# Kernel tuning notes

Hardware: AMD Instinct MI355X
Metric: run time of the kernel (lower is better)

Reference implementation:

```python
import jax, jax.numpy as jnp
import numpy as np

EPS = 1e-5

def _conv_bn_relu(x, w, gamma, beta):
    # x: [B, C, N], w: [O, C] (1x1 conv, no bias)
    y = jnp.einsum('oc,bcn->bon', w, x)
    # BatchNorm1d in training mode: per-channel stats over (B, N)
    mean = jnp.mean(y, axis=(0, 2), keepdims=True)
    var = jnp.var(y, axis=(0, 2), keepdims=True)
    yhat = (y - mean) * jax.lax.rsqrt(var + EPS)
    return jax.nn.relu(gamma[None, :, None] * yhat + beta[None, :, None])


def setup_inputs() -> dict:
    key = jax.random.key(0)
    ks = jax.random.split(key, 8)
    B, C, N, Cr = 4, 256, 4096, 32
    x = jax.random.normal(ks[0], (B, C, N), dtype=jnp.float32)
    w1 = jax.random.normal(ks[1], (Cr, C), dtype=jnp.float32) * (1.0 / np.sqrt(C))
    w2 = jax.random.normal(ks[2], (Cr, C), dtype=jnp.float32) * (1.0 / np.sqrt(C))
    w3 = jax.random.normal(ks[3], (C, C), dtype=jnp.float32) * (1.0 / np.sqrt(C))
    g1 = 1.0 + 0.1 * jax.random.normal(ks[4], (Cr,), dtype=jnp.float32)
    b1 = 0.1 * jax.random.normal(ks[5], (Cr,), dtype=jnp.float32)
    g2 = 1.0 + 0.1 * jax.random.normal(ks[6], (Cr,), dtype=jnp.float32)
    b2 = 0.1 * jax.random.normal(ks[7], (Cr,), dtype=jnp.float32)
    g3 = jnp.ones((C,), dtype=jnp.float32)
    b3 = jnp.zeros((C,), dtype=jnp.float32)
    return {'x': x, 'w1': w1, 'w2': w2, 'w3': w3,
            'g1': g1, 'b1': b1, 'g2': g2, 'b2': b2, 'g3': g3, 'b3': b3}


def reference(x, w1, w2, w3, g1, b1, g2, b2, g3, b3):
    # a: [B, N, Cr] (queries), k: [B, Cr, N] (keys)
    a = _conv_bn_relu(x, w1, g1, b1).transpose(0, 2, 1)
    k = _conv_bn_relu(x, w2, g2, b2)
    # s[b, n, m] = softmax_m(sum_c a[b,n,c] * k[b,c,m])
    s = jax.nn.softmax(jnp.einsum('bnc,bcm->bnm', a, k), axis=-1)
    d = _conv_bn_relu(x, w3, g3, b3)  # [B, C, N]
    # out = x + d @ s^T : out[b,c,m] = sum_n d[b,c,n] * s[m,n]
    out = x + jnp.einsum('bcn,bmn->bcm', d, s)
    return out
```

## Files before the change

### kernel.cpp

```cpp
#include <hip/hip_runtime.h>
#include <cstddef>
#include <cstdint>

#define B_ 4
#define C_ 256
#define N_ 4096
#define KF_OFF_B  ((size_t)1024 * 1024)
#define DF_OFF_B  ((size_t)2 * 1024 * 1024)
#define SUM_OFF_B ((size_t)10 * 1024 * 1024)
#define ML_OFF_B  (SUM_OFF_B + 1280 * 4)
#define XH_OFF_B  (ML_OFF_B + 524288)
#define XL_OFF_B  (XH_OFF_B + (size_t)8 * 1024 * 1024)
#define WH_OFF_B  (XL_OFF_B + (size_t)8 * 1024 * 1024)
#define WL_OFF_B  (WH_OFF_B + 163840)
#define LOG2E 1.4426950408889634f

typedef unsigned short bfraw;
typedef __attribute__((ext_vector_type(8))) short short8;
typedef __attribute__((ext_vector_type(4))) float float4v;
typedef __attribute__((ext_vector_type(4))) bfraw bfraw4;

__device__ inline bfraw f2bf(float f) {
    union { float f; uint32_t u; } c; c.f = f;
    uint32_t u = c.u;
    u += 0x7fffu + ((u >> 16) & 1u);
    return (bfraw)(u >> 16);
}
__device__ inline float bf2f(bfraw h) {
    union { uint32_t u; float f; } c; c.u = ((uint32_t)h) << 16;
    return c.f;
}
#if __has_builtin(__builtin_amdgcn_exp2f)
__device__ inline float EXP2(float x) { return __builtin_amdgcn_exp2f(x); }
#else
__device__ inline float EXP2(float x) { return exp2f(x); }
#endif
__device__ inline uint32_t pack2(float a, float b) {
    union { float f; uint32_t u; } ca, cb; ca.f = a; cb.f = b;
#if __has_builtin(__builtin_amdgcn_perm)
    return __builtin_amdgcn_perm(cb.u + 0x8000u, ca.u + 0x8000u, 0x07060302u);
#else
    return ((ca.u + 0x8000u) >> 16) | ((cb.u + 0x8000u) & 0xffff0000u);
#endif
}

__global__ void zero_kernel(float* __restrict__ sums) {
    for (int i = threadIdx.x; i < 640; i += 256) sums[i] = 0.f;
}

__global__ __launch_bounds__(256) void wsplit_kernel(
    const float* __restrict__ w1, const float* __restrict__ w2,
    const float* __restrict__ w3, uint8_t* __restrict__ wsb)
{
    bfraw* wh = (bfraw*)(wsb + WH_OFF_B);
    bfraw* wl = (bfraw*)(wsb + WL_OFF_B);
    int idx4 = (blockIdx.x * 256 + threadIdx.x) * 4;
    int ch = idx4 >> 8, k = idx4 & 255;
    const float* wr = (ch < 32) ? (w1 + ch * C_)
                      : (ch < 64) ? (w2 + (ch - 32) * C_)
                                  : (w3 + (ch - 64) * C_);
    float4 v = *(const float4*)&wr[k];
    float va[4] = {v.x, v.y, v.z, v.w};
    bfraw4 h, l;
#pragma unroll
    for (int j = 0; j < 4; ++j) {
        h[j] = f2bf(va[j]);
        l[j] = f2bf(va[j] - bf2f(h[j]));
    }
    *(bfraw4*)&wh[idx4] = h;
    *(bfraw4*)&wl[idx4] = l;
}

__global__ __launch_bounds__(256) void xtsplit_kernel(
    const float* __restrict__ x, uint8_t* __restrict__ wsb)
{
    __shared__ float Ls[64][65];
    bfraw* xh = (bfraw*)(wsb + XH_OFF_B);
    bfraw* xl = (bfraw*)(wsb + XL_OFF_B);
    const int id = blockIdx.x;
    const int b  = id >> 8;
    const int c0 = ((id >> 6) & 3) << 6;
    const int n0 = (id & 63) << 6;
    const int t  = threadIdx.x;
    {
        int cl = t >> 4, nc = (t & 15) << 2;
#pragma unroll
        for (int i = 0; i < 4; ++i) {
            float4 v = *(const float4*)&x[((size_t)b * C_ + c0 + cl + i * 16) * N_ + n0 + nc];
            Ls[cl + i * 16][nc + 0] = v.x;
            Ls[cl + i * 16][nc + 1] = v.y;
            Ls[cl + i * 16][nc + 2] = v.z;
            Ls[cl + i * 16][nc + 3] = v.w;
        }
    }
    __syncthreads();
    int nl = t >> 2, seg = t & 3;
    bfraw hb[16], lb[16];
#pragma unroll
    for (int j = 0; j < 16; ++j) {
        float v = Ls[seg * 16 + j][nl];
        bfraw h = f2bf(v);
        hb[j] = h;
        lb[j] = f2bf(v - bf2f(h));
    }
    size_t base = ((size_t)b * N_ + n0 + nl) * 256 + c0 + seg * 16;
    *(short8*)&xh[base]     = *(short8*)&hb[0];
    *(short8*)&xh[base + 8] = *(short8*)&hb[8];
    *(short8*)&xl[base]     = *(short8*)&lb[0];
    *(short8*)&xl[base + 8] = *(short8*)&lb[8];
}

__global__ __launch_bounds__(256, 2) void ygemm_kernel(uint8_t* __restrict__ wsb)
{
    const bfraw* xh = (const bfraw*)(wsb + XH_OFF_B);
    const bfraw* xl = (const bfraw*)(wsb + XL_OFF_B);
    const bfraw* wh = (const bfraw*)(wsb + WH_OFF_B);
    const bfraw* wl = (const bfraw*)(wsb + WL_OFF_B);
    bfraw* qf  = (bfraw*)wsb;
    bfraw* kfp = (bfraw*)(wsb + KF_OFF_B);
    bfraw* dfp = (bfraw*)(wsb + DF_OFF_B);
    float* sums  = (float*)(wsb + SUM_OFF_B);
    float* sumsq = sums + 320;
    __shared__ float redS[4][64], redQ[4][64];

    const int bx = blockIdx.x;
    const int by = blockIdx.y;
    const int b  = bx >> 5;
    const int n0 = (bx << 7) & (N_ - 1);
    const int t = threadIdx.x, w = t >> 6, l = t & 63, lq = l & 15, lg = l >> 4;
    const int nw = n0 + w * 32;

    float4v acc[4][2];
#pragma unroll
    for (int i = 0; i < 4; ++i)
#pragma unroll
        for (int j = 0; j < 2; ++j) acc[i][j] = (float4v){0.f, 0.f, 0.f, 0.f};

    for (int s = 0; s < 8; ++s) {
        const int k0 = s * 32;
        short8 ah[4], al[4], bh[2], bl[2];
#pragma unroll
        for (int ct = 0; ct < 4; ++ct) {
            size_t off = (size_t)(by * 64 + ct * 16 + lq) * 256 + k0 + lg * 8;
            ah[ct] = *(const short8*)&wh[off];
            al[ct] = *(const short8*)&wl[off];
        }
#pragma unroll
        for (int nt = 0; nt < 2; ++nt) {
            size_t off = ((size_t)b * N_ + nw + nt * 16 + lq) * 256 + k0 + lg * 8;
            bh[nt] = *(const short8*)&xh[off];
            bl[nt] = *(const short8*)&xl[off];
        }
#pragma unroll
        for (int ct = 0; ct < 4; ++ct)
#pragma unroll
            for (int nt = 0; nt < 2; ++nt) {
                acc[ct][nt] = __builtin_amdgcn_mfma_f32_16x16x32_bf16(ah[ct], bh[nt], acc[ct][nt], 0, 0, 0);
                acc[ct][nt] = __builtin_amdgcn_mfma_f32_16x16x32_bf16(al[ct], bh[nt], acc[ct][nt], 0, 0, 0);
                acc[ct][nt] = __builtin_amdgcn_mfma_f32_16x16x32_bf16(ah[ct], bl[nt], acc[ct][nt], 0, 0, 0);
            }
    }
#pragma unroll
    for (int ct = 0; ct < 4; ++ct) {
        float sv[4], qv[4];
#pragma unroll
        for (int r = 0; r < 4; ++r) {
            float a0 = acc[ct][0][r], a1 = acc[ct][1][r];
            sv[r] = a0 + a1;
            qv[r] = a0 * a0 + a1 * a1;
#pragma unroll
            for (int m = 1; m < 16; m <<= 1) {
                sv[r] += __shfl_xor(sv[r], m);
                qv[r] += __shfl_xor(qv[r], m);
            }
        }
        if (lq == 0) {
#pragma unroll
            for (int r = 0; r < 4; ++r) {
                redS[w][ct * 16 + lg * 4 + r] = sv[r];
                redQ[w][ct * 16 + lg * 4 + r] = qv[r];
            }
        }
    }
    __syncthreads();
    if (t < 64) {
        float s = redS[0][t] + redS[1][t] + redS[2][t] + redS[3][t];
        float q = redQ[0][t] + redQ[1][t] + redQ[2][t] + redQ[3][t];
        atomicAdd(&sums[by * 64 + t], s);
        atomicAdd(&sumsq[by * 64 + t], q);
    }
    if (by == 0) {
#pragma unroll
        for (int ct = 0; ct < 4; ++ct)
#pragma unroll
            for (int nt = 0; nt < 2; ++nt)
#pragma unroll
                for (int r = 0; r < 4; ++r) {
                    int c = ct * 16 + lg * 4 + r;
                    int n = nw + nt * 16 + lq;
                    size_t addr = ((size_t)(b << 8) + (n >> 4)) * 512
                                + (size_t)(((n & 15) | (((c >> 3) & 3) << 4)) << 3) + (c & 7);
                    bfraw v = f2bf(acc[ct][nt][r]);
                    if (c < 32) qf[addr] = v; else kfp[addr] = v;
                }
    } else {
#pragma unroll
        for (int ct = 0; ct < 4; ++ct)
#pragma unroll
            for (int nt = 0; nt < 2; ++nt)
#pragma unroll
                for (int r = 0; r < 4; ++r) {
                    int cg = (by - 1) * 64 + ct * 16 + lg * 4 + r;
                    int n = nw + nt * 16 + lq;
                    size_t addr = (((size_t)(b << 4) + (cg >> 4)) * 128 + (n >> 5)) * 512
                                + (size_t)(((cg & 15) | (((n >> 3) & 3) << 4)) << 3) + (n & 7);
                    dfp[addr] = f2bf(acc[ct][nt][r]);
                }
    }
}

__global__ void finalize_kernel(
    const float* __restrict__ g1, const float* __restrict__ b1,
    const float* __restrict__ g2, const float* __restrict__ b2,
    const float* __restrict__ g3, const float* __restrict__ b3,
    float* __restrict__ sums)
{
    int ch = threadIdx.x;
    if (ch >= 320) return;
    const float inv = 1.0f / (float)(B_ * N_);
    float mean = sums[ch] * inv;
    float var = sums[320 + ch] * inv - mean * mean;
    float g, bb;
    if (ch < 32)      { g = g1[ch];      bb = b1[ch]; }
    else if (ch < 64) { g = g2[ch - 32]; bb = b2[ch - 32]; }
    else              { g = g3[ch - 64]; bb = b3[ch - 64]; }
    float sc = g * rsqrtf(var + 1e-5f);
    float bi = bb - sc * mean;
    if (ch < 32) { sc *= LOG2E; bi *= LOG2E; }
    sums[640 + ch] = sc;
    sums[960 + ch] = bi;
}

__global__ __launch_bounds__(256) void affine_kernel(uint8_t* __restrict__ wsb)
{
    bfraw* base = (bfraw*)wsb;
    const float* sc = (const float*)(wsb + SUM_OFF_B) + 640;
    const float* bi = sc + 320;
    size_t i8 = ((size_t)blockIdx.x * 256 + threadIdx.x) * 8;
    bfraw4 v0 = *(bfraw4*)&base[i8];
    bfraw4 v1 = *(bfraw4*)&base[i8 + 4];
    if (i8 < 1048576) {
        int ch0 = (((int)(i8 >> 7)) & 3) * 8 + ((i8 < 524288) ? 0 : 32);
        float4 s0 = *(const float4*)&sc[ch0];
        float4 s1 = *(const float4*)&sc[ch0 + 4];
        float4 c0 = *(const float4*)&bi[ch0];
        float4 c1 = *(const float4*)&bi[ch0 + 4];
        float sa[8] = {s0.x, s0.y, s0.z, s0.w, s1.x, s1.y, s1.z, s1.w};
        float ca[8] = {c0.x, c0.y, c0.z, c0.w, c1.x, c1.y, c1.z, c1.w};
#pragma unroll
        for (int j = 0; j < 4; ++j) {
            v0[j] = f2bf(fmaxf(0.f, fmaf(sa[j],     bf2f(v0[j]), ca[j])));
            v1[j] = f2bf(fmaxf(0.f, fmaf(sa[j + 4], bf2f(v1[j]), ca[j + 4])));
        }
    } else {
        size_t rel = i8 - 1048576;
        int ch = 64 + (((int)(rel >> 16)) & 15) * 16 + (((int)(rel >> 3)) & 15);
        float s = sc[ch], b = bi[ch];
#pragma unroll
        for (int j = 0; j < 4; ++j) {
            v0[j] = f2bf(fmaxf(0.f, fmaf(s, bf2f(v0[j]), b)));
            v1[j] = f2bf(fmaxf(0.f, fmaf(s, bf2f(v1[j]), b)));
        }
    }
    *(bfraw4*)&base[i8] = v0;
    *(bfraw4*)&base[i8 + 4] = v1;
}

__global__ __launch_bounds__(256, 4) void mlpass_kernel(uint8_t* __restrict__ wsb)
{
    const bfraw* qf  = (const bfraw*)wsb;
    const bfraw* kfp = (const bfraw*)(wsb + KF_OFF_B);
    float* mpart = (float*)(wsb + ML_OFF_B);
    float* lpart = mpart + 65536;
    const int id = blockIdx.x;
    const int b = id & 3;
    const int ks = (id >> 2) & 3;
    const int n0q = (id >> 4) << 6;
    const int tid = threadIdx.x;
    const int w = tid >> 6, l = tid & 63, lq = l & 15, lg = l >> 4;
    const short8 qfrag = *(const short8*)&qf[((size_t)(b * 256 + (n0q >> 4) + w)) * 512 + l * 8];

    float mx = -1e30f, sum = 0.f;
    const int tbeg = b * 256 + ks * 64;
    for (int tk = tbeg; tk < tbeg + 64; tk += 8) {
        float4v st[8];
#pragma unroll
        for (int kt = 0; kt < 8; ++kt) {
            short8 kf = *(const short8*)&kfp[((size_t)(tk + kt)) * 512 + l * 8];
            float4v z = {0.f, 0.f, 0.f, 0.f};
            st[kt] = __builtin_amdgcn_mfma_f32_16x16x32_bf16(kf, qfrag, z, 0, 0, 0);
        }
        float m1 = st[0][0];
#pragma unroll
        for (int kt = 0; kt < 8; ++kt)
#pragma unroll
            for (int r = 0; r < 4; ++r) m1 = fmaxf(m1, st[kt][r]);
        float nm = fmaxf(mx, m1);
        float ae = 0.f;
#pragma unroll
        for (int kt = 0; kt < 8; ++kt)
#pragma unroll
            for (int r = 0; r < 4; ++r) ae += EXP2(st[kt][r] - nm);
        sum = sum * EXP2(mx - nm) + ae;
        mx = nm;
    }
#pragma unroll
    for (int m = 16; m < 64; m <<= 1) {
        float mo = __shfl_xor(mx, m);
        float so = __shfl_xor(sum, m);
        float nm = fmaxf(mx, mo);
        sum = sum * EXP2(mx - nm) + so * EXP2(mo - nm);
        mx = nm;
    }
    if (lg == 0) {
        int idx = ks * 16384 + b * N_ + n0q + w * 16 + lq;
        mpart[idx] = mx;
        lpart[idx] = sum;
    }
}

__global__ __launch_bounds__(256, 4) void flash_kernel(
    const float* __restrict__ x, const uint8_t* __restrict__ wsb,
    float* __restrict__ out)
{
    const bfraw* qf  = (const bfraw*)wsb;
    const bfraw* kfp = (const bfraw*)(wsb + KF_OFF_B);
    const bfraw* dfp = (const bfraw*)(wsb + DF_OFF_B);
    const float* mpart = (const float*)(wsb + ML_OFF_B);
    const float* lpart = mpart + 65536;
    __shared__ bfraw Pl[2][32 * 128];

    const int id  = blockIdx.x;
    const int b   = id & 3;
    const int hf  = (id >> 2) & 1;
    const int n0q = (id >> 3) << 5;
    const int tid = threadIdx.x;
    const int w   = tid >> 6;
    const int l   = tid & 63;
    const int lq  = l & 15;
    const int lg  = l >> 4;
    const int sw  = lq & 7;
    const int qt_loc = w >> 1;
    const int ks_loc = w & 1;
    const int ctg0 = hf * 8 + w;
    const int ctg1 = hf * 8 + 4 + w;

    const short8 qfrag = *(const short8*)&qf[((size_t)(b * 256 + (n0q >> 4) + qt_loc)) * 512 + l * 8];
    float mlq;
    {
        int qi = b * N_ + n0q + qt_loc * 16 + lq;
        float M = -1e30f, ms[4], ls[4];
#pragma unroll
        for (int s = 0; s < 4; ++s) {
            ms[s] = mpart[s * 16384 + qi];
            ls[s] = lpart[s * 16384 + qi];
            M = fmaxf(M, ms[s]);
        }
        float L = 0.f;
#pragma unroll
        for (int s = 0; s < 4; ++s) L += ls[s] * EXP2(ms[s] - M);
        mlq = M + __log2f(L);
    }

    float4v acc[2][2];
#pragma unroll
    for (int i = 0; i < 2; ++i)
#pragma unroll
        for (int j = 0; j < 2; ++j) acc[i][j] = (float4v){0.f, 0.f, 0.f, 0.f};

    short8 kfr[4], dfr[2][4];
#pragma unroll
    for (int kt = 0; kt < 4; ++kt)
        kfr[kt] = *(const short8*)&kfp[((size_t)(b * 256 + ks_loc * 4 + kt)) * 512 + l * 8];
#pragma unroll
    for (int ch = 0; ch < 4; ++ch) {
        dfr[0][ch] = *(const short8*)&dfp[(((size_t)(b * 16 + ctg0)) * 128 + ch) * 512 + l * 8];
        dfr[1][ch] = *(const short8*)&dfp[(((size_t)(b * 16 + ctg1)) * 128 + ch) * 512 + l * 8];
    }

    const int qrow = qt_loc * 16 + lq;
    for (int it = 0; it < 32; ++it) {
        const int ib = it & 1;
        const int nit = (it + 1) & 31;
        float4v st[4];
#pragma unroll
        for (int kt = 0; kt < 4; ++kt) {
            float4v z = {0.f, 0.f, 0.f, 0.f};
            st[kt] = __builtin_amdgcn_mfma_f32_16x16x32_bf16(kfr[kt], qfrag, z, 0, 0, 0);
        }
#pragma unroll
        for (int kt = 0; kt < 4; ++kt)
            kfr[kt] = *(const short8*)&kfp[((size_t)(b * 256 + nit * 8 + ks_loc * 4 + kt)) * 512 + l * 8];
#pragma unroll
        for (int kt = 0; kt < 4; ++kt) {
            float e0 = EXP2(st[kt][0] - mlq);
            float e1 = EXP2(st[kt][1] - mlq);
            float e2 = EXP2(st[kt][2] - mlq);
            float e3 = EXP2(st[kt][3] - mlq);
            uint2 pd = {pack2(e0, e1), pack2(e2, e3)};
            int g = (2 * (ks_loc * 4 + kt) + (lg >> 1)) ^ sw;
            *(uint2*)&Pl[ib][qrow * 128 + g * 8 + (lg & 1) * 4] = pd;
        }
        __syncthreads();
#pragma unroll
        for (int ch = 0; ch < 4; ++ch) {
            short8 bfr[2];
#pragma unroll
            for (int qt = 0; qt < 2; ++qt) {
                int g = (ch * 4 + lg) ^ sw;
                bfr[qt] = *(const short8*)&Pl[ib][(qt * 16 + lq) * 128 + g * 8];
            }
            acc[0][0] = __builtin_amdgcn_mfma_f32_16x16x32_bf16(dfr[0][ch], bfr[0], acc[0][0], 0, 0, 0);
            acc[0][1] = __builtin_amdgcn_mfma_f32_16x16x32_bf16(dfr[0][ch], bfr[1], acc[0][1], 0, 0, 0);
            acc[1][0] = __builtin_amdgcn_mfma_f32_16x16x32_bf16(dfr[1][ch], bfr[0], acc[1][0], 0, 0, 0);
            acc[1][1] = __builtin_amdgcn_mfma_f32_16x16x32_bf16(dfr[1][ch], bfr[1], acc[1][1], 0, 0, 0);
            dfr[0][ch] = *(const short8*)&dfp[(((size_t)(b * 16 + ctg0)) * 128 + nit * 4 + ch) * 512 + l * 8];
            dfr[1][ch] = *(const short8*)&dfp[(((size_t)(b * 16 + ctg1)) * 128 + nit * 4 + ch) * 512 + l * 8];
        }
    }
#pragma unroll
    for (int ct = 0; ct < 2; ++ct) {
        int ctg = ct ? ctg1 : ctg0;
#pragma unroll
        for (int r = 0; r < 4; ++r) {
            int c = ctg * 16 + lg * 4 + r;
            size_t base = ((size_t)b * C_ + c) * N_ + n0q;
#pragma unroll
            for (int qt = 0; qt < 2; ++qt) {
                size_t idx = base + qt * 16 + lq;
                out[idx] = x[idx] + acc[ct][qt][r];
            }
        }
    }
}

extern "C" void kernel_launch(void* const* d_in, const int* in_sizes, int n_in,
                              void* d_out, int out_size, void* d_ws, size_t ws_size,
                              hipStream_t stream) {
    (void)in_sizes; (void)n_in; (void)out_size; (void)ws_size;
    const float* x  = (const float*)d_in[0];
    const float* w1 = (const float*)d_in[1];
    const float* w2 = (const float*)d_in[2];
    const float* w3 = (const float*)d_in[3];
    const float* g1 = (const float*)d_in[4];
    const float* b1 = (const float*)d_in[5];
    const float* g2 = (const float*)d_in[6];
    const float* b2 = (const float*)d_in[7];
    const float* g3 = (const float*)d_in[8];
    const float* b3 = (const float*)d_in[9];
    uint8_t* wsb = (uint8_t*)d_ws;
    float* sums = (float*)(wsb + SUM_OFF_B);
    float* outp = (float*)d_out;

    zero_kernel<<<1, 256, 0, stream>>>(sums);
    wsplit_kernel<<<80, 256, 0, stream>>>(w1, w2, w3, wsb);
    xtsplit_kernel<<<1024, 256, 0, stream>>>(x, wsb);
    ygemm_kernel<<<dim3(128, 5), 256, 0, stream>>>(wsb);
    finalize_kernel<<<1, 320, 0, stream>>>(g1, b1, g2, b2, g3, b3, sums);
    affine_kernel<<<2560, 256, 0, stream>>>(wsb);
    mlpass_kernel<<<1024, 256, 0, stream>>>(wsb);
    flash_kernel<<<1024, 256, 0, stream>>>(x, wsb, outp);
}
```

Measured before the change: 211.2 us.

## Double query tile per flash block to reuse K/D fragments

Each flash block now handles 64 queries instead of 32. Every loaded K and D fragment feeds twice as many MFMAs, and the grid halves to 512 blocks. The log-sum-exp offset is folded into the MFMA accumulator init so the separate subtract before exp2 goes away, and s_setprio is raised around the MFMA burst. In exchange, register use and LDS usage double (launch bounds drop to 2) and there are fewer blocks to hide latency.

```diff
diff --git a/kernel.cpp b/kernel.cpp
--- a/kernel.cpp
+++ b/kernel.cpp
@@ -329,7 +329,7 @@
     }
 }
 
-__global__ __launch_bounds__(256, 4) void flash_kernel(
+__global__ __launch_bounds__(256, 2) void flash_kernel(
     const float* __restrict__ x, const uint8_t* __restrict__ wsb,
     float* __restrict__ out)
 {
@@ -338,27 +338,30 @@
     const bfraw* dfp = (const bfraw*)(wsb + DF_OFF_B);
     const float* mpart = (const float*)(wsb + ML_OFF_B);
     const float* lpart = mpart + 65536;
-    __shared__ bfraw Pl[2][32 * 128];
+    __shared__ bfraw Pl[2][64 * 128];
 
     const int id  = blockIdx.x;
     const int b   = id & 3;
     const int hf  = (id >> 2) & 1;
-    const int n0q = (id >> 3) << 5;
+    const int n0q = (id >> 3) << 6;
     const int tid = threadIdx.x;
     const int w   = tid >> 6;
     const int l   = tid & 63;
     const int lq  = l & 15;
     const int lg  = l >> 4;
     const int sw  = lq & 7;
-    const int qt_loc = w >> 1;
+    const int qp  = w >> 1;
     const int ks_loc = w & 1;
     const int ctg0 = hf * 8 + w;
     const int ctg1 = hf * 8 + 4 + w;
 
-    const short8 qfrag = *(const short8*)&qf[((size_t)(b * 256 + (n0q >> 4) + qt_loc)) * 512 + l * 8];
-    float mlq;
-    {
-        int qi = b * N_ + n0q + qt_loc * 16 + lq;
+    const short8 qfragA = *(const short8*)&qf[((size_t)(b * 256 + (n0q >> 4) + 2 * qp)) * 512 + l * 8];
+    const short8 qfragB = *(const short8*)&qf[((size_t)(b * 256 + (n0q >> 4) + 2 * qp + 1)) * 512 + l * 8];
+
+    float mlqA, mlqB;
+#pragma unroll
+    for (int qs = 0; qs < 2; ++qs) {
+        int qi = b * N_ + n0q + (2 * qp + qs) * 16 + lq;
         float M = -1e30f, ms[4], ls[4];
 #pragma unroll
         for (int s = 0; s < 4; ++s) {
@@ -369,14 +372,17 @@
         float L = 0.f;
 #pragma unroll
         for (int s = 0; s < 4; ++s) L += ls[s] * EXP2(ms[s] - M);
-        mlq = M + __log2f(L);
-    }
-
-    float4v acc[2][2];
+        float v = M + __log2f(L);
+        if (qs == 0) mlqA = v; else mlqB = v;
+    }
+    const float4v zA = {-mlqA, -mlqA, -mlqA, -mlqA};
+    const float4v zB = {-mlqB, -mlqB, -mlqB, -mlqB};
+
+    float4v acc[2][4];
 #pragma unroll
     for (int i = 0; i < 2; ++i)
 #pragma unroll
-        for (int j = 0; j < 2; ++j) acc[i][j] = (float4v){0.f, 0.f, 0.f, 0.f};
+        for (int j = 0; j < 4; ++j) acc[i][j] = (float4v){0.f, 0.f, 0.f, 0.f};
 
     short8 kfr[4], dfr[2][4];
 #pragma unroll
@@ -388,42 +394,55 @@
         dfr[1][ch] = *(const short8*)&dfp[(((size_t)(b * 16 + ctg1)) * 128 + ch) * 512 + l * 8];
     }
 
-    const int qrow = qt_loc * 16 + lq;
+    const int qrowA = (2 * qp) * 16 + lq;
+    const int qrowB = (2 * qp + 1) * 16 + lq;
     for (int it = 0; it < 32; ++it) {
         const int ib = it & 1;
         const int nit = (it + 1) & 31;
-        float4v st[4];
+        float4v stA[4], stB[4];
 #pragma unroll
         for (int kt = 0; kt < 4; ++kt) {
-            float4v z = {0.f, 0.f, 0.f, 0.f};
-            st[kt] = __builtin_amdgcn_mfma_f32_16x16x32_bf16(kfr[kt], qfrag, z, 0, 0, 0);
+            stA[kt] = __builtin_amdgcn_mfma_f32_16x16x32_bf16(kfr[kt], qfragA, zA, 0, 0, 0);
+            stB[kt] = __builtin_amdgcn_mfma_f32_16x16x32_bf16(kfr[kt], qfragB, zB, 0, 0, 0);
         }
 #pragma unroll
         for (int kt = 0; kt < 4; ++kt)
             kfr[kt] = *(const short8*)&kfp[((size_t)(b * 256 + nit * 8 + ks_loc * 4 + kt)) * 512 + l * 8];
 #pragma unroll
         for (int kt = 0; kt < 4; ++kt) {
-            float e0 = EXP2(st[kt][0] - mlq);
-            float e1 = EXP2(st[kt][1] - mlq);
-            float e2 = EXP2(st[kt][2] - mlq);
-            float e3 = EXP2(st[kt][3] - mlq);
-            uint2 pd = {pack2(e0, e1), pack2(e2, e3)};
             int g = (2 * (ks_loc * 4 + kt) + (lg >> 1)) ^ sw;
-            *(uint2*)&Pl[ib][qrow * 128 + g * 8 + (lg & 1) * 4] = pd;
+            {
+                float e0 = EXP2(stA[kt][0]);
+                float e1 = EXP2(stA[kt][1]);
+                float e2 = EXP2(stA[kt][2]);
+                float e3 = EXP2(stA[kt][3]);
+                uint2 pd = {pack2(e0, e1), pack2(e2, e3)};
+                *(uint2*)&Pl[ib][qrowA * 128 + g * 8 + (lg & 1) * 4] = pd;
+            }
+            {
+                float e0 = EXP2(stB[kt][0]);
+                float e1 = EXP2(stB[kt][1]);
+                float e2 = EXP2(stB[kt][2]);
+                float e3 = EXP2(stB[kt][3]);
+                uint2 pd = {pack2(e0, e1), pack2(e2, e3)};
+                *(uint2*)&Pl[ib][qrowB * 128 + g * 8 + (lg & 1) * 4] = pd;
+            }
         }
         __syncthreads();
 #pragma unroll
         for (int ch = 0; ch < 4; ++ch) {
-            short8 bfr[2];
-#pragma unroll
-            for (int qt = 0; qt < 2; ++qt) {
-                int g = (ch * 4 + lg) ^ sw;
+            short8 bfr[4];
+            int g = (ch * 4 + lg) ^ sw;
+#pragma unroll
+            for (int qt = 0; qt < 4; ++qt)
                 bfr[qt] = *(const short8*)&Pl[ib][(qt * 16 + lq) * 128 + g * 8];
-            }
-            acc[0][0] = __builtin_amdgcn_mfma_f32_16x16x32_bf16(dfr[0][ch], bfr[0], acc[0][0], 0, 0, 0);
-            acc[0][1] = __builtin_amdgcn_mfma_f32_16x16x32_bf16(dfr[0][ch], bfr[1], acc[0][1], 0, 0, 0);
-            acc[1][0] = __builtin_amdgcn_mfma_f32_16x16x32_bf16(dfr[1][ch], bfr[0], acc[1][0], 0, 0, 0);
-            acc[1][1] = __builtin_amdgcn_mfma_f32_16x16x32_bf16(dfr[1][ch], bfr[1], acc[1][1], 0, 0, 0);
+            __builtin_amdgcn_s_setprio(1);
+#pragma unroll
+            for (int qt = 0; qt < 4; ++qt) {
+                acc[0][qt] = __builtin_amdgcn_mfma_f32_16x16x32_bf16(dfr[0][ch], bfr[qt], acc[0][qt], 0, 0, 0);
+                acc[1][qt] = __builtin_amdgcn_mfma_f32_16x16x32_bf16(dfr[1][ch], bfr[qt], acc[1][qt], 0, 0, 0);
+            }
+            __builtin_amdgcn_s_setprio(0);
             dfr[0][ch] = *(const short8*)&dfp[(((size_t)(b * 16 + ctg0)) * 128 + nit * 4 + ch) * 512 + l * 8];
             dfr[1][ch] = *(const short8*)&dfp[(((size_t)(b * 16 + ctg1)) * 128 + nit * 4 + ch) * 512 + l * 8];
         }
@@ -436,7 +455,7 @@
             int c = ctg * 16 + lg * 4 + r;
             size_t base = ((size_t)b * C_ + c) * N_ + n0q;
 #pragma unroll
-            for (int qt = 0; qt < 2; ++qt) {
+            for (int qt = 0; qt < 4; ++qt) {
                 size_t idx = base + qt * 16 + lq;
                 out[idx] = x[idx] + acc[ct][qt][r];
             }
@@ -469,5 +488,5 @@
     finalize_kernel<<<1, 320, 0, stream>>>(g1, b1, g2, b2, g3, b3, sums);
     affine_kernel<<<2560, 256, 0, stream>>>(wsb);
     mlpass_kernel<<<1024, 256, 0, stream>>>(wsb);
-    flash_kernel<<<1024, 256, 0, stream>>>(x, wsb, outp);
-}
+    flash_kernel<<<512, 256, 0, stream>>>(x, wsb, outp);
+}
```

Result: faster. 197.4 us (-6.5%).
